# Optimization experiments

Measured on AMD Instinct MI355X. Metric: run time of the kernel, lower is better.

Reference implementation:

```python
import jax, jax.numpy as jnp
import numpy as np

N = 100000      # nodes
E = 1600000     # edges (avg degree 16)
D = 128         # in = hid = out dim


def setup_inputs() -> dict:
    key = jax.random.key(0)
    ks = jax.random.split(key, 7)
    x = jax.random.normal(ks[0], (N, D), dtype=jnp.float32)
    src = jax.random.randint(ks[1], (E,), 0, N, dtype=jnp.int32)
    dst = jax.random.randint(ks[2], (E,), 0, N, dtype=jnp.int32)
    s = 1.0 / np.sqrt(2 * D)  # torch Linear default init bound
    W0 = jax.random.uniform(ks[3], (D, 2 * D), jnp.float32, -s, s)
    b0 = jax.random.uniform(ks[4], (D,), jnp.float32, -s, s)
    W1 = jax.random.uniform(ks[5], (D, 2 * D), jnp.float32, -s, s)
    b1 = jax.random.uniform(ks[6], (D,), jnp.float32, -s, s)
    return {"x": x, "src": src, "dst": dst, "W0": W0, "b0": b0, "W1": W1, "b1": b1}


def graph_conv_left(x, src, dst):
    """DGL GraphConv(norm='left', weight=False, bias=False):
    h_v = sum_{(u->v) in E} x_u / max(outdeg(u), 1)."""
    n = x.shape[0]
    deg = jax.ops.segment_sum(jnp.ones_like(src, dtype=x.dtype), src, num_segments=n)
    deg = jnp.maximum(deg, 1.0)
    msgs = (x / deg[:, None])[src]          # [E, D] gather of normalized src feats
    return jax.ops.segment_sum(msgs, dst, num_segments=n)  # [N, D] scatter-add


def reference(x, src, dst, W0, b0, W1, b1):
    # layer 0: concat(self, agg) -> linear -> relu
    h = jnp.concatenate([x, graph_conv_left(x, src, dst)], axis=1)  # [N, 2D]
    h = jax.nn.relu(h @ W0.T + b0)                                  # [N, D]
    # layer 1 (output): concat -> linear (no relu)
    out = jnp.concatenate([h, graph_conv_left(h, src, dst)], axis=1) @ W1.T + b1
    return out
```

## Files before the change

kernel.cpp:

```cpp
#include <hip/hip_runtime.h>
#include <hip/hip_fp16.h>

#define DIM 128
#define CAP 64
#define BW_LOG 8
#define BW_NODES 256
#define CHUNK_P 4096
#define KCELL 40
#define MAXCHUNK 512
#define WSTRIDE 264

typedef _Float16 f16x8 __attribute__((ext_vector_type(8)));
typedef float f32x4 __attribute__((ext_vector_type(4)));
typedef unsigned int uint;

__global__ __launch_bounds__(512) void k_front(const int* __restrict__ src,
                                               const int* __restrict__ dst,
                                               uint* __restrict__ dbuf,
                                               uint* __restrict__ sbuf,
                                               uint* __restrict__ cntD,
                                               uint* __restrict__ cntS,
                                               const float* __restrict__ W0,
                                               const float* __restrict__ W1,
                                               const float* __restrict__ x,
                                               __half* __restrict__ Wh0,
                                               __half* __restrict__ Wh1,
                                               __half* __restrict__ fh,
                                               int E, int NB, int nchunk, int nquadX) {
    if ((int)blockIdx.x >= nchunk) {
        int i = ((int)blockIdx.x - nchunk) * 512 + threadIdx.x;
        const float* in; __half* out; int q;
        if (i < 8192)        { in = W0; out = Wh0; q = i; }
        else if (i < 16384)  { in = W1; out = Wh1; q = i - 8192; }
        else {
            q = i - 16384;
            if (q >= nquadX) return;
            in = x; out = fh;
        }
        float4 v = ((const float4*)in)[q];
        __half2* o = (__half2*)out;
        o[q * 2]     = __floats2half2_rn(v.x, v.y);
        o[q * 2 + 1] = __floats2half2_rn(v.z, v.w);
        return;
    }
    extern __shared__ uint smem[];
    uint* rb    = smem;
    uint* cells = smem + NB;
    int blk = blockIdx.x;
    int e0 = blk * CHUNK_P;

    int4 sv[2], dv[2];
    bool ok[2];
#pragma unroll
    for (int q = 0; q < 2; ++q) {
        int i4 = (e0 >> 2) + q * 512 + (int)threadIdx.x;
        int e = i4 << 2;
        ok[q] = (e < E);
        if (ok[q]) {
            sv[q] = ((const int4*)src)[i4];
            dv[q] = ((const int4*)dst)[i4];
        }
    }

    const int KQ = KCELL / 4;
    int nq = NB * KQ;

    for (int i = threadIdx.x; i < NB; i += 512) rb[i] = 0;
    __syncthreads();
#pragma unroll
    for (int q = 0; q < 2; ++q) {
        if (!ok[q]) continue;
        int ds[4] = {dv[q].x, dv[q].y, dv[q].z, dv[q].w};
        int ss[4] = {sv[q].x, sv[q].y, sv[q].z, sv[q].w};
#pragma unroll
        for (int k = 0; k < 4; ++k) {
            uint d = (uint)ds[k];
            uint bd = d >> BW_LOG;
            uint r = atomicAdd(&rb[bd], 1);
            if (r < KCELL)
                cells[bd * KCELL + r] = ((d & (BW_NODES - 1)) << 17) | (uint)ss[k];
        }
    }
    __syncthreads();
    for (int u = threadIdx.x; u < nq; u += 512) {
        int bucket = u / KQ;
        int s4 = u - bucket * KQ;
        ((uint4*)dbuf)[((size_t)bucket * nchunk + blk) * KQ + s4] = ((const uint4*)cells)[u];
    }
    for (int i = threadIdx.x; i < NB; i += 512) {
        uint c = rb[i];
        cntD[(uint)i * nchunk + blk] = c < KCELL ? c : KCELL;
    }
    __syncthreads();

    for (int i = threadIdx.x; i < NB; i += 512) rb[i] = 0;
    __syncthreads();
#pragma unroll
    for (int q = 0; q < 2; ++q) {
        if (!ok[q]) continue;
        int ss[4] = {sv[q].x, sv[q].y, sv[q].z, sv[q].w};
#pragma unroll
        for (int k = 0; k < 4; ++k) {
            uint s = (uint)ss[k];
            uint bs = s >> BW_LOG;
            uint r = atomicAdd(&rb[bs], 1);
            if (r < KCELL)
                cells[bs * KCELL + r] = s;
        }
    }
    __syncthreads();
    for (int u = threadIdx.x; u < nq; u += 512) {
        int bucket = u / KQ;
        int s4 = u - bucket * KQ;
        ((uint4*)sbuf)[((size_t)bucket * nchunk + blk) * KQ + s4] = ((const uint4*)cells)[u];
    }
    for (int i = threadIdx.x; i < NB; i += 512) {
        uint c = rb[i];
        cntS[(uint)i * nchunk + blk] = c < KCELL ? c : KCELL;
    }
}

__global__ __launch_bounds__(512) void k_build(const uint* __restrict__ dbuf,
                                               const uint* __restrict__ cntD,
                                               const uint* __restrict__ sbuf,
                                               const uint* __restrict__ cntS,
                                               int* __restrict__ edge_pad,
                                               int* __restrict__ cnt,
                                               float* __restrict__ invd,
                                               int N, int NB, int nchunk) {
    __shared__ uint mcell[MAXCHUNK];
    __shared__ uint cur[BW_NODES];
    __shared__ int  img[128 * CAP];
    int gid = blockIdx.x;
    if (gid < NB) {
        int b = gid;
        for (int c = threadIdx.x; c < nchunk; c += 512)
            mcell[c] = cntD[(uint)b * nchunk + c];
        uint base = (uint)b * nchunk * KCELL;
        int total = nchunk * KCELL;
        int node0 = b << BW_LOG;
        for (int g = 0; g < 2; ++g) {
            int l0 = g << 7;
            for (int i = threadIdx.x; i < 128; i += 512) cur[i] = 0;
            __syncthreads();
            uint v[4]; bool val[4];
            for (int sb = 0; sb < total; sb += 2048) {
#pragma unroll
                for (int q = 0; q < 4; ++q) {
                    int s = sb + q * 512 + (int)threadIdx.x;
                    val[q] = false;
                    if (s < total) {
                        int c = s / KCELL;
                        int j = s - c * KCELL;
                        if ((uint)j < mcell[c]) { val[q] = true; v[q] = dbuf[base + s]; }
                    }
                }
#pragma unroll
                for (int q = 0; q < 4; ++q) {
                    if (val[q]) {
                        uint local = v[q] >> 17;
                        if ((int)(local >> 7) == g) {
                            uint slot = atomicAdd(&cur[local - l0], 1);
                            if (slot < CAP)
                                img[(local - l0) * CAP + slot] = (int)(v[q] & 0x1FFFFu);
                        }
                    }
                }
            }
            __syncthreads();
            int4* gp = (int4*)&edge_pad[(size_t)(node0 + l0) * CAP];
            const int4* lp = (const int4*)img;
            for (int i = threadIdx.x; i < 128 * CAP / 4; i += 512) {
                int row = i >> 4;
                if (node0 + l0 + row < N) gp[i] = lp[i];
            }
            for (int i = threadIdx.x; i < 128; i += 512) {
                int node = node0 + l0 + i;
                if (node < N) cnt[node] = (int)(cur[i] < CAP ? cur[i] : CAP);
            }
            __syncthreads();
        }
    } else {
        int b = gid - NB;
        for (int c = threadIdx.x; c < nchunk; c += 512)
            mcell[c] = cntS[(uint)b * nchunk + c];
        for (int i = threadIdx.x; i < BW_NODES; i += 512) cur[i] = 0;
        __syncthreads();
        uint base = (uint)b * nchunk * KCELL;
        int total = nchunk * KCELL;
        uint v[4]; bool val[4];
        for (int sb = 0; sb < total; sb += 2048) {
#pragma unroll
            for (int q = 0; q < 4; ++q) {
                int s = sb + q * 512 + (int)threadIdx.x;
                val[q] = false;
                if (s < total) {
                    int c = s / KCELL;
                    int j = s - c * KCELL;
                    if ((uint)j < mcell[c]) { val[q] = true; v[q] = sbuf[base + s]; }
                }
            }
#pragma unroll
            for (int q = 0; q < 4; ++q)
                if (val[q]) atomicAdd(&cur[v[q] & (BW_NODES - 1)], 1);
        }
        __syncthreads();
        int node0 = b << BW_LOG;
        for (int i = threadIdx.x; i < BW_NODES; i += 512) {
            int node = node0 + i;
            if (node < N) {
                uint d = cur[i];
                invd[node] = 1.0f / (float)(d > 1u ? d : 1u);
            }
        }
    }
}

__global__ __launch_bounds__(256) void k_gather(const __half* __restrict__ feat,
                                                const float* __restrict__ invd,
                                                const int* __restrict__ edge_pad,
                                                const int* __restrict__ cnt_arr,
                                                __half* __restrict__ agg, int n) {
    int v = blockIdx.x * 4 + (threadIdx.x >> 6);
    int lane = threadIdx.x & 63;
    int quad = lane >> 4;
    int lq   = lane & 15;
    if (v >= n) return;
    int cnt = cnt_arr[v];
    if (cnt > CAP) cnt = CAP;

    int u_lane = 0;
    float w_lane = 0.f;
    if (lane < cnt) {
        u_lane = edge_pad[(size_t)v * CAP + lane];
        w_lane = invd[u_lane];
    }

    float acc[8] = {0.f, 0.f, 0.f, 0.f, 0.f, 0.f, 0.f, 0.f};
    int cntUp = (cnt + 7) & ~7;
    for (int j = 0; j < cntUp; j += 8) {
        int   ua = __shfl(u_lane, j + quad);
        float wa = __shfl(w_lane, j + quad);
        int   ub = __shfl(u_lane, j + 4 + quad);
        float wb = __shfl(w_lane, j + 4 + quad);
        uint4 ra = *(const uint4*)&feat[(size_t)ua * 128 + lq * 8];
        uint4 rb = *(const uint4*)&feat[(size_t)ub * 128 + lq * 8];
        const __half2* pa = (const __half2*)&ra;
        const __half2* pb = (const __half2*)&rb;
#pragma unroll
        for (int i = 0; i < 4; ++i) {
            float2 fa = __half22float2(pa[i]);
            float2 fb = __half22float2(pb[i]);
            acc[2 * i]     = fmaf(fa.x, wa, acc[2 * i]);
            acc[2 * i + 1] = fmaf(fa.y, wa, acc[2 * i + 1]);
            acc[2 * i]     = fmaf(fb.x, wb, acc[2 * i]);
            acc[2 * i + 1] = fmaf(fb.y, wb, acc[2 * i + 1]);
        }
    }
#pragma unroll
    for (int off = 16; off <= 32; off <<= 1) {
#pragma unroll
        for (int i = 0; i < 8; ++i) acc[i] += __shfl_xor(acc[i], off);
    }
    if (quad == 0) {
        __half2 o[4];
#pragma unroll
        for (int i = 0; i < 4; ++i) o[i] = __floats2half2_rn(acc[2 * i], acc[2 * i + 1]);
        *(uint4*)&agg[(size_t)v * 128 + lq * 8] = *(const uint4*)o;
    }
}

template <bool RELU, bool OUT16>
__global__ __launch_bounds__(256) void k_gemm_f16(const _Float16* __restrict__ A0,
                                                  const _Float16* __restrict__ A1,
                                                  const _Float16* __restrict__ Wh,
                                                  const float* __restrict__ bias,
                                                  float* __restrict__ out32,
                                                  _Float16* __restrict__ out16,
                                                  int n_rows) {
    __shared__ _Float16 Ws[64 * WSTRIDE];
    int tid  = threadIdx.x;
    int wave = tid >> 6;
    int lane = tid & 63;
    int quad = lane >> 4;
    int l16  = lane & 15;

    int u = blockIdx.x;
    int full = (int)gridDim.x & ~15;
    int mb, half;
    if (u < full) { mb = (u >> 4) * 8 + (u & 7); half = (u >> 3) & 1; }
    else {
        int rem = ((int)gridDim.x >> 1) - (full >> 1);
        int t = u - full;
        mb = (full >> 1) + t % rem;
        half = t / rem;
    }
    int n0 = half * 64;
    int m0 = mb * 128 + wave * 32;

#pragma unroll
    for (int i = 0; i < 8; ++i) {
        int chunk = i * 256 + tid;
        int r = chunk >> 5;
        int c = (chunk & 31) * 8;
        *(f16x8*)&Ws[r * WSTRIDE + c] = *(const f16x8*)&Wh[(n0 + r) * 256 + c];
    }
    __syncthreads();

    f32x4 acc[2][4] = {};

    int ra = m0 + l16;
    int rb = m0 + 16 + l16;
    size_t r0 = (size_t)(ra < n_rows ? ra : 0);
    size_t r1 = (size_t)(rb < n_rows ? rb : 0);

#pragma unroll
    for (int ks = 0; ks < 8; ++ks) {
        int k0 = ks * 32;
        const _Float16* Ab = (k0 < 128) ? A0 : A1;
        int kk = (k0 & 127) + quad * 8;
        f16x8 a0 = *(const f16x8*)&Ab[r0 * 128 + kk];
        f16x8 a1 = *(const f16x8*)&Ab[r1 * 128 + kk];
        f16x8 b[4];
#pragma unroll
        for (int t = 0; t < 4; ++t)
            b[t] = *(const f16x8*)&Ws[(t * 16 + l16) * WSTRIDE + k0 + quad * 8];
#pragma unroll
        for (int t = 0; t < 4; ++t) {
            acc[0][t] = __builtin_amdgcn_mfma_f32_16x16x32_f16(a0, b[t], acc[0][t], 0, 0, 0);
            acc[1][t] = __builtin_amdgcn_mfma_f32_16x16x32_f16(a1, b[t], acc[1][t], 0, 0, 0);
        }
    }

#pragma unroll
    for (int t = 0; t < 4; ++t) {
        int col = n0 + t * 16 + l16;
        float bv = bias[col];
#pragma unroll
        for (int g = 0; g < 2; ++g) {
#pragma unroll
            for (int r = 0; r < 4; ++r) {
                int row = m0 + g * 16 + quad * 4 + r;
                if (row < n_rows) {
                    float v = acc[g][t][r] + bv;
                    if (RELU) v = fmaxf(v, 0.f);
                    if (OUT16) out16[(size_t)row * 128 + col] = (_Float16)v;
                    else       out32[(size_t)row * 128 + col] = v;
                }
            }
        }
    }
}

extern "C" void kernel_launch(void* const* d_in, const int* in_sizes, int n_in,
                              void* d_out, int out_size, void* d_ws, size_t ws_size,
                              hipStream_t stream) {
    const float* x  = (const float*)d_in[0];
    const int*   src = (const int*)d_in[1];
    const int*   dst = (const int*)d_in[2];
    const float* W0 = (const float*)d_in[3];
    const float* b0 = (const float*)d_in[4];
    const float* W1 = (const float*)d_in[5];
    const float* b1 = (const float*)d_in[6];
    int N = in_sizes[0] / DIM;
    int E = in_sizes[1];
    float* out = (float*)d_out;
    int NB = (N + BW_NODES - 1) >> BW_LOG;
    int nchunk = (E + CHUNK_P - 1) / CHUNK_P;
    size_t ncell = (size_t)NB * nchunk;
    size_t cellWords = ncell * KCELL;

    char* p = (char*)d_ws;
    uint* cntDc = (uint*)p; p += (ncell * 4 + 63) & ~(size_t)63;
    uint* cntSc = (uint*)p; p += (ncell * 4 + 63) & ~(size_t)63;
    int*   edge_pad = (int*)p;   p += (size_t)N * CAP * 4;
    int*   cnt  = (int*)p;  p += ((size_t)N * 4 + 63) & ~(size_t)63;
    float* invd = (float*)p; p += ((size_t)N * 4 + 63) & ~(size_t)63;
    char*  uni = p;
    size_t featB = (size_t)N * DIM * 2;
    size_t cellB = cellWords * 4;
    size_t uniSz = cellB > featB ? cellB : featB;
    p += (uniSz + 63) & ~(size_t)63;
    uint*   dbuf = (uint*)uni;
    __half* aggh = (__half*)uni;
    __half* fh   = (__half*)p; p += featB;
    char*  uni2 = p; p += (uniSz + 63) & ~(size_t)63;
    uint*   sbuf = (uint*)uni2;
    __half* hh   = (__half*)uni2;
    __half* Wh0  = (__half*)p; p += 128 * 256 * 2;
    __half* Wh1  = (__half*)p; p += 128 * 256 * 2;
    (void)ws_size; (void)n_in; (void)out_size;

    int nquadX = N * DIM / 4;
    int gP = (16384 + nquadX + 511) / 512;
    size_t shScatter = (size_t)(NB + NB * KCELL) * 4;
    k_front<<<nchunk + gP, 512, shScatter, stream>>>(src, dst, dbuf, sbuf, cntDc, cntSc,
                                                     W0, W1, x, Wh0, Wh1, fh,
                                                     E, NB, nchunk, nquadX);

    k_build<<<2 * NB, 512, 0, stream>>>(dbuf, cntDc, sbuf, cntSc,
                                        edge_pad, cnt, invd, N, NB, nchunk);

    int gG = (N + 3) / 4;
    int gM = 2 * ((N + 127) / 128);

    k_gather<<<gG, 256, 0, stream>>>(fh, invd, edge_pad, cnt, aggh, N);
    k_gemm_f16<true, true><<<gM, 256, 0, stream>>>((const _Float16*)fh, (const _Float16*)aggh,
                                                   (const _Float16*)Wh0, b0,
                                                   nullptr, (_Float16*)hh, N);

    k_gather<<<gG, 256, 0, stream>>>(hh, invd, edge_pad, cnt, aggh, N);
    k_gemm_f16<false, false><<<gM, 256, 0, stream>>>((const _Float16*)hh, (const _Float16*)aggh,
                                                     (const _Float16*)Wh1, b1,
                                                     out, nullptr, N);
}
```

Measured before the change: 316.6 us.

## Fuse neighbor gather with MFMA linear layer, prepermute weights into fragment layout

Merges the per-node gather kernel and the GEMM kernel into one kernel per layer: each wave aggregates 16 nodes into shared memory and then runs MFMA over the concatenated self and aggregate features against all 128 output columns. Weights are pre-permuted at conversion time into the MFMA B-fragment order, so they are read straight from global memory without LDS staging. This removes the aggregate buffer round trip through global memory and two launches. In exchange, gather parallelism per block drops because each wave handles its 16 nodes serially, and every wave re-reads the full weight matrix from global or cache.

New measurement: 348.3 us. 1.1x slower.

```diff
diff --git a/kernel.cpp b/kernel.cpp
--- a/kernel.cpp
+++ b/kernel.cpp
@@ -8,7 +8,6 @@
 #define CHUNK_P 4096
 #define KCELL 40
 #define MAXCHUNK 512
-#define WSTRIDE 264
 
 typedef _Float16 f16x8 __attribute__((ext_vector_type(8)));
 typedef float f32x4 __attribute__((ext_vector_type(4)));
@@ -23,22 +22,35 @@
                                                const float* __restrict__ W0,
                                                const float* __restrict__ W1,
                                                const float* __restrict__ x,
-                                               __half* __restrict__ Wh0,
-                                               __half* __restrict__ Wh1,
+                                               _Float16* __restrict__ Wr0,
+                                               _Float16* __restrict__ Wr1,
                                                __half* __restrict__ fh,
                                                int E, int NB, int nchunk, int nquadX) {
     if ((int)blockIdx.x >= nchunk) {
         int i = ((int)blockIdx.x - nchunk) * 512 + threadIdx.x;
-        const float* in; __half* out; int q;
-        if (i < 8192)        { in = W0; out = Wh0; q = i; }
-        else if (i < 16384)  { in = W1; out = Wh1; q = i - 8192; }
-        else {
-            q = i - 16384;
-            if (q >= nquadX) return;
-            in = x; out = fh;
-        }
-        float4 v = ((const float4*)in)[q];
-        __half2* o = (__half2*)out;
+        if (i < 8192) {
+            const float* W = (i < 4096) ? W0 : W1;
+            _Float16* Wr  = (i < 4096) ? Wr0 : Wr1;
+            int j = i & 4095;
+            int f = j >> 6;
+            int ln = j & 63;
+            int ks = f >> 3, t = f & 7;
+            int col = t * 16 + (ln & 15);
+            int k0 = ks * 32 + (ln >> 4) * 8;
+            const float* wsrc = W + (size_t)col * 256 + k0;
+            float4 va = *(const float4*)wsrc;
+            float4 vb = *(const float4*)(wsrc + 4);
+            __half2* o = (__half2*)(Wr + ((size_t)f * 64 + ln) * 8);
+            o[0] = __floats2half2_rn(va.x, va.y);
+            o[1] = __floats2half2_rn(va.z, va.w);
+            o[2] = __floats2half2_rn(vb.x, vb.y);
+            o[3] = __floats2half2_rn(vb.z, vb.w);
+            return;
+        }
+        int q = i - 8192;
+        if (q >= nquadX) return;
+        float4 v = ((const float4*)x)[q];
+        __half2* o = (__half2*)fh;
         o[q * 2]     = __floats2half2_rn(v.x, v.y);
         o[q * 2 + 1] = __floats2half2_rn(v.z, v.w);
         return;
@@ -216,137 +228,97 @@
     }
 }
 
-__global__ __launch_bounds__(256) void k_gather(const __half* __restrict__ feat,
-                                                const float* __restrict__ invd,
-                                                const int* __restrict__ edge_pad,
-                                                const int* __restrict__ cnt_arr,
-                                                __half* __restrict__ agg, int n) {
-    int v = blockIdx.x * 4 + (threadIdx.x >> 6);
-    int lane = threadIdx.x & 63;
-    int quad = lane >> 4;
-    int lq   = lane & 15;
-    if (v >= n) return;
-    int cnt = cnt_arr[v];
-    if (cnt > CAP) cnt = CAP;
-
-    int u_lane = 0;
-    float w_lane = 0.f;
-    if (lane < cnt) {
-        u_lane = edge_pad[(size_t)v * CAP + lane];
-        w_lane = invd[u_lane];
-    }
-
-    float acc[8] = {0.f, 0.f, 0.f, 0.f, 0.f, 0.f, 0.f, 0.f};
-    int cntUp = (cnt + 7) & ~7;
-    for (int j = 0; j < cntUp; j += 8) {
-        int   ua = __shfl(u_lane, j + quad);
-        float wa = __shfl(w_lane, j + quad);
-        int   ub = __shfl(u_lane, j + 4 + quad);
-        float wb = __shfl(w_lane, j + 4 + quad);
-        uint4 ra = *(const uint4*)&feat[(size_t)ua * 128 + lq * 8];
-        uint4 rb = *(const uint4*)&feat[(size_t)ub * 128 + lq * 8];
-        const __half2* pa = (const __half2*)&ra;
-        const __half2* pb = (const __half2*)&rb;
-#pragma unroll
-        for (int i = 0; i < 4; ++i) {
-            float2 fa = __half22float2(pa[i]);
-            float2 fb = __half22float2(pb[i]);
-            acc[2 * i]     = fmaf(fa.x, wa, acc[2 * i]);
-            acc[2 * i + 1] = fmaf(fa.y, wa, acc[2 * i + 1]);
-            acc[2 * i]     = fmaf(fb.x, wb, acc[2 * i]);
-            acc[2 * i + 1] = fmaf(fb.y, wb, acc[2 * i + 1]);
-        }
-    }
-#pragma unroll
-    for (int off = 16; off <= 32; off <<= 1) {
-#pragma unroll
-        for (int i = 0; i < 8; ++i) acc[i] += __shfl_xor(acc[i], off);
-    }
-    if (quad == 0) {
-        __half2 o[4];
-#pragma unroll
-        for (int i = 0; i < 4; ++i) o[i] = __floats2half2_rn(acc[2 * i], acc[2 * i + 1]);
-        *(uint4*)&agg[(size_t)v * 128 + lq * 8] = *(const uint4*)o;
-    }
-}
-
 template <bool RELU, bool OUT16>
-__global__ __launch_bounds__(256) void k_gemm_f16(const _Float16* __restrict__ A0,
-                                                  const _Float16* __restrict__ A1,
-                                                  const _Float16* __restrict__ Wh,
-                                                  const float* __restrict__ bias,
-                                                  float* __restrict__ out32,
-                                                  _Float16* __restrict__ out16,
-                                                  int n_rows) {
-    __shared__ _Float16 Ws[64 * WSTRIDE];
+__global__ __launch_bounds__(256) void k_fused(const __half* __restrict__ feat,
+                                               const float* __restrict__ invd,
+                                               const int* __restrict__ edge_pad,
+                                               const int* __restrict__ cnt_arr,
+                                               const _Float16* __restrict__ Wr,
+                                               const float* __restrict__ bias,
+                                               float* __restrict__ out32,
+                                               _Float16* __restrict__ out16,
+                                               int n_rows) {
+    __shared__ _Float16 agg[64 * 136];
     int tid  = threadIdx.x;
     int wave = tid >> 6;
     int lane = tid & 63;
     int quad = lane >> 4;
-    int l16  = lane & 15;
-
-    int u = blockIdx.x;
-    int full = (int)gridDim.x & ~15;
-    int mb, half;
-    if (u < full) { mb = (u >> 4) * 8 + (u & 7); half = (u >> 3) & 1; }
-    else {
-        int rem = ((int)gridDim.x >> 1) - (full >> 1);
-        int t = u - full;
-        mb = (full >> 1) + t % rem;
-        half = t / rem;
-    }
-    int n0 = half * 64;
-    int m0 = mb * 128 + wave * 32;
-
-#pragma unroll
-    for (int i = 0; i < 8; ++i) {
-        int chunk = i * 256 + tid;
-        int r = chunk >> 5;
-        int c = (chunk & 31) * 8;
-        *(f16x8*)&Ws[r * WSTRIDE + c] = *(const f16x8*)&Wh[(n0 + r) * 256 + c];
-    }
-    __syncthreads();
-
-    f32x4 acc[2][4] = {};
-
-    int ra = m0 + l16;
-    int rb = m0 + 16 + l16;
-    size_t r0 = (size_t)(ra < n_rows ? ra : 0);
-    size_t r1 = (size_t)(rb < n_rows ? rb : 0);
-
+    int lq   = lane & 15;
+    int rowbase = blockIdx.x * 64 + wave * 16;
+
+    for (int nn = 0; nn < 16; ++nn) {
+        int v = rowbase + nn;
+        if (v >= n_rows) break;
+        int cnt = cnt_arr[v];
+        if (cnt > CAP) cnt = CAP;
+        int u_lane = 0;
+        float w_lane = 0.f;
+        if (lane < cnt) {
+            u_lane = edge_pad[(size_t)v * CAP + lane];
+            w_lane = invd[u_lane];
+        }
+        float acc[8] = {0.f, 0.f, 0.f, 0.f, 0.f, 0.f, 0.f, 0.f};
+        int cntUp = (cnt + 7) & ~7;
+        for (int j = 0; j < cntUp; j += 8) {
+            int   ua = __shfl(u_lane, j + quad);
+            float wa = __shfl(w_lane, j + quad);
+            int   ub = __shfl(u_lane, j + 4 + quad);
+            float wb = __shfl(w_lane, j + 4 + quad);
+            uint4 ra = *(const uint4*)&feat[(size_t)ua * 128 + lq * 8];
+            uint4 rb = *(const uint4*)&feat[(size_t)ub * 128 + lq * 8];
+            const __half2* pa = (const __half2*)&ra;
+            const __half2* pb = (const __half2*)&rb;
+#pragma unroll
+            for (int i = 0; i < 4; ++i) {
+                float2 fa = __half22float2(pa[i]);
+                float2 fb = __half22float2(pb[i]);
+                acc[2 * i]     = fmaf(fa.x, wa, acc[2 * i]);
+                acc[2 * i + 1] = fmaf(fa.y, wa, acc[2 * i + 1]);
+                acc[2 * i]     = fmaf(fb.x, wb, acc[2 * i]);
+                acc[2 * i + 1] = fmaf(fb.y, wb, acc[2 * i + 1]);
+            }
+        }
+#pragma unroll
+        for (int off = 16; off <= 32; off <<= 1) {
+#pragma unroll
+            for (int i = 0; i < 8; ++i) acc[i] += __shfl_xor(acc[i], off);
+        }
+        if (quad == 0) {
+            __half2 o[4];
+#pragma unroll
+            for (int i = 0; i < 4; ++i) o[i] = __floats2half2_rn(acc[2 * i], acc[2 * i + 1]);
+            *(uint4*)&agg[(wave * 16 + nn) * 136 + lq * 8] = *(const uint4*)o;
+        }
+    }
+
+    f32x4 acc[8] = {};
+    int myrow = rowbase + lq;
+    size_t ar = (size_t)(myrow < n_rows ? myrow : 0);
+    const _Float16* fp = (const _Float16*)feat;
+    int aggoff = (wave * 16 + lq) * 136 + quad * 8;
 #pragma unroll
     for (int ks = 0; ks < 8; ++ks) {
-        int k0 = ks * 32;
-        const _Float16* Ab = (k0 < 128) ? A0 : A1;
-        int kk = (k0 & 127) + quad * 8;
-        f16x8 a0 = *(const f16x8*)&Ab[r0 * 128 + kk];
-        f16x8 a1 = *(const f16x8*)&Ab[r1 * 128 + kk];
-        f16x8 b[4];
-#pragma unroll
-        for (int t = 0; t < 4; ++t)
-            b[t] = *(const f16x8*)&Ws[(t * 16 + l16) * WSTRIDE + k0 + quad * 8];
-#pragma unroll
-        for (int t = 0; t < 4; ++t) {
-            acc[0][t] = __builtin_amdgcn_mfma_f32_16x16x32_f16(a0, b[t], acc[0][t], 0, 0, 0);
-            acc[1][t] = __builtin_amdgcn_mfma_f32_16x16x32_f16(a1, b[t], acc[1][t], 0, 0, 0);
-        }
-    }
-
-#pragma unroll
-    for (int t = 0; t < 4; ++t) {
-        int col = n0 + t * 16 + l16;
+        f16x8 a;
+        if (ks < 4) a = *(const f16x8*)&fp[ar * 128 + ks * 32 + quad * 8];
+        else        a = *(const f16x8*)&agg[aggoff + (ks - 4) * 32];
+#pragma unroll
+        for (int t = 0; t < 8; ++t) {
+            f16x8 b = *(const f16x8*)&Wr[((size_t)((ks * 8 + t) * 64 + lane)) * 8];
+            acc[t] = __builtin_amdgcn_mfma_f32_16x16x32_f16(a, b, acc[t], 0, 0, 0);
+        }
+    }
+#pragma unroll
+    for (int t = 0; t < 8; ++t) {
+        int col = t * 16 + lq;
         float bv = bias[col];
 #pragma unroll
-        for (int g = 0; g < 2; ++g) {
-#pragma unroll
-            for (int r = 0; r < 4; ++r) {
-                int row = m0 + g * 16 + quad * 4 + r;
-                if (row < n_rows) {
-                    float v = acc[g][t][r] + bv;
-                    if (RELU) v = fmaxf(v, 0.f);
-                    if (OUT16) out16[(size_t)row * 128 + col] = (_Float16)v;
-                    else       out32[(size_t)row * 128 + col] = v;
-                }
+        for (int r = 0; r < 4; ++r) {
+            int row = rowbase + quad * 4 + r;
+            if (row < n_rows) {
+                float v = acc[t][r] + bv;
+                if (RELU) v = fmaxf(v, 0.f);
+                if (OUT16) out16[(size_t)row * 128 + col] = (_Float16)v;
+                else       out32[(size_t)row * 128 + col] = v;
             }
         }
     }
@@ -376,41 +348,34 @@
     int*   edge_pad = (int*)p;   p += (size_t)N * CAP * 4;
     int*   cnt  = (int*)p;  p += ((size_t)N * 4 + 63) & ~(size_t)63;
     float* invd = (float*)p; p += ((size_t)N * 4 + 63) & ~(size_t)63;
-    char*  uni = p;
     size_t featB = (size_t)N * DIM * 2;
     size_t cellB = cellWords * 4;
     size_t uniSz = cellB > featB ? cellB : featB;
-    p += (uniSz + 63) & ~(size_t)63;
+    char*  uni = p; p += (uniSz + 63) & ~(size_t)63;
     uint*   dbuf = (uint*)uni;
-    __half* aggh = (__half*)uni;
     __half* fh   = (__half*)p; p += featB;
     char*  uni2 = p; p += (uniSz + 63) & ~(size_t)63;
     uint*   sbuf = (uint*)uni2;
     __half* hh   = (__half*)uni2;
-    __half* Wh0  = (__half*)p; p += 128 * 256 * 2;
-    __half* Wh1  = (__half*)p; p += 128 * 256 * 2;
+    _Float16* Wr0 = (_Float16*)p; p += 64 * 64 * 8 * 2;
+    _Float16* Wr1 = (_Float16*)p; p += 64 * 64 * 8 * 2;
     (void)ws_size; (void)n_in; (void)out_size;
 
     int nquadX = N * DIM / 4;
-    int gP = (16384 + nquadX + 511) / 512;
+    int gP = (8192 + nquadX + 511) / 512;
     size_t shScatter = (size_t)(NB + NB * KCELL) * 4;
     k_front<<<nchunk + gP, 512, shScatter, stream>>>(src, dst, dbuf, sbuf, cntDc, cntSc,
-                                                     W0, W1, x, Wh0, Wh1, fh,
+                                                     W0, W1, x, Wr0, Wr1, fh,
                                                      E, NB, nchunk, nquadX);
 
     k_build<<<2 * NB, 512, 0, stream>>>(dbuf, cntDc, sbuf, cntSc,
                                         edge_pad, cnt, invd, N, NB, nchunk);
 
-    int gG = (N + 3) / 4;
-    int gM = 2 * ((N + 127) / 128);
-
-    k_gather<<<gG, 256, 0, stream>>>(fh, invd, edge_pad, cnt, aggh, N);
-    k_gemm_f16<true, true><<<gM, 256, 0, stream>>>((const _Float16*)fh, (const _Float16*)aggh,
-                                                   (const _Float16*)Wh0, b0,
-                                                   nullptr, (_Float16*)hh, N);
-
-    k_gather<<<gG, 256, 0, stream>>>(hh, invd, edge_pad, cnt, aggh, N);
-    k_gemm_f16<false, false><<<gM, 256, 0, stream>>>((const _Float16*)hh, (const _Float16*)aggh,
-                                                     (const _Float16*)Wh1, b1,
-                                                     out, nullptr, N);
+    int gF = (N + 63) / 64;
+
+    k_fused<true, true><<<gF, 256, 0, stream>>>(fh, invd, edge_pad, cnt,
+                                                Wr0, b0, nullptr, (_Float16*)hh, N);
+
+    k_fused<false, false><<<gF, 256, 0, stream>>>(hh, invd, edge_pad, cnt,
+                                                  Wr1, b1, out, nullptr, N);
 }
```

## Compress source-degree cells to bytes and compute full output width per GEMM block

Applied to the files above, without the earlier changes.

The source-bucket cells now hold only the low 8 bits of each node id (one byte per entry, padded to 48 per cell). This cuts the global traffic the front kernel writes and the degree-counting build pass reads, and the build pass unpacks four entries per word. The GEMM kernel now has each block compute both 64-column halves of the output, loading the A rows once into registers and restaging W in shared memory twice. That halves A reads and the grid size, at the cost of higher register pressure and an extra barrier-separated weight load.

Result: slower. 328.5 us (+3.8%).

```diff
diff --git a/kernel.cpp b/kernel.cpp
--- a/kernel.cpp
+++ b/kernel.cpp
@@ -7,12 +7,14 @@
 #define BW_NODES 256
 #define CHUNK_P 4096
 #define KCELL 40
+#define KCB   48
 #define MAXCHUNK 512
 #define WSTRIDE 264
 
 typedef _Float16 f16x8 __attribute__((ext_vector_type(8)));
 typedef float f32x4 __attribute__((ext_vector_type(4)));
 typedef unsigned int uint;
+typedef unsigned char uchar;
 
 __global__ __launch_bounds__(512) void k_front(const int* __restrict__ src,
                                                const int* __restrict__ dst,
@@ -44,8 +46,10 @@
         return;
     }
     extern __shared__ uint smem[];
-    uint* rb    = smem;
-    uint* cells = smem + NB;
+    int NBa = (NB + 3) & ~3;
+    uint*  rb     = smem;
+    uint*  cells  = smem + NBa;
+    uchar* cellsB = (uchar*)(smem + NBa);
     int blk = blockIdx.x;
     int e0 = blk * CHUNK_P;
 
@@ -105,14 +109,16 @@
             uint bs = s >> BW_LOG;
             uint r = atomicAdd(&rb[bs], 1);
             if (r < KCELL)
-                cells[bs * KCELL + r] = s;
+                cellsB[bs * KCB + r] = (uchar)(s & (BW_NODES - 1));
         }
     }
     __syncthreads();
-    for (int u = threadIdx.x; u < nq; u += 512) {
-        int bucket = u / KQ;
-        int s4 = u - bucket * KQ;
-        ((uint4*)sbuf)[((size_t)bucket * nchunk + blk) * KQ + s4] = ((const uint4*)cells)[u];
+    const int KQS = KCB / 16;
+    int nqS = NB * KQS;
+    for (int u = threadIdx.x; u < nqS; u += 512) {
+        int bucket = u / KQS;
+        int s4 = u - bucket * KQS;
+        ((uint4*)sbuf)[((size_t)bucket * nchunk + blk) * KQS + s4] = ((const uint4*)cellsB)[u];
     }
     for (int i = threadIdx.x; i < NB; i += 512) {
         uint c = rb[i];
@@ -186,23 +192,33 @@
             mcell[c] = cntS[(uint)b * nchunk + c];
         for (int i = threadIdx.x; i < BW_NODES; i += 512) cur[i] = 0;
         __syncthreads();
-        uint base = (uint)b * nchunk * KCELL;
-        int total = nchunk * KCELL;
-        uint v[4]; bool val[4];
-        for (int sb = 0; sb < total; sb += 2048) {
+        const uint* sbU = sbuf + (size_t)b * nchunk * (KCB / 4);
+        int totalU = nchunk * (KCB / 4);
+        uint w[4]; int cc[4], jb[4]; bool val[4];
+        for (int su = 0; su < totalU; su += 2048) {
 #pragma unroll
             for (int q = 0; q < 4; ++q) {
-                int s = sb + q * 512 + (int)threadIdx.x;
+                int s = su + q * 512 + (int)threadIdx.x;
                 val[q] = false;
-                if (s < total) {
-                    int c = s / KCELL;
-                    int j = s - c * KCELL;
-                    if ((uint)j < mcell[c]) { val[q] = true; v[q] = sbuf[base + s]; }
+                if (s < totalU) {
+                    int c = s / (KCB / 4);
+                    int j = (s - c * (KCB / 4)) * 4;
+                    if ((uint)j < mcell[c]) {
+                        val[q] = true; w[q] = sbU[s]; cc[q] = c; jb[q] = j;
+                    }
                 }
             }
 #pragma unroll
-            for (int q = 0; q < 4; ++q)
-                if (val[q]) atomicAdd(&cur[v[q] & (BW_NODES - 1)], 1);
+            for (int q = 0; q < 4; ++q) {
+                if (val[q]) {
+                    uint m = mcell[cc[q]];
+                    uint ww = w[q];
+#pragma unroll
+                    for (int i = 0; i < 4; ++i)
+                        if ((uint)(jb[q] + i) < m)
+                            atomicAdd(&cur[(ww >> (8 * i)) & 255u], 1);
+                }
+            }
         }
         __syncthreads();
         int node0 = b << BW_LOG;
@@ -284,68 +300,67 @@
     int lane = tid & 63;
     int quad = lane >> 4;
     int l16  = lane & 15;
-
-    int u = blockIdx.x;
-    int full = (int)gridDim.x & ~15;
-    int mb, half;
-    if (u < full) { mb = (u >> 4) * 8 + (u & 7); half = (u >> 3) & 1; }
-    else {
-        int rem = ((int)gridDim.x >> 1) - (full >> 1);
-        int t = u - full;
-        mb = (full >> 1) + t % rem;
-        half = t / rem;
-    }
-    int n0 = half * 64;
-    int m0 = mb * 128 + wave * 32;
-
-#pragma unroll
-    for (int i = 0; i < 8; ++i) {
-        int chunk = i * 256 + tid;
-        int r = chunk >> 5;
-        int c = (chunk & 31) * 8;
-        *(f16x8*)&Ws[r * WSTRIDE + c] = *(const f16x8*)&Wh[(n0 + r) * 256 + c];
-    }
-    __syncthreads();
-
-    f32x4 acc[2][4] = {};
+    int m0 = blockIdx.x * 128 + wave * 32;
 
     int ra = m0 + l16;
     int rb = m0 + 16 + l16;
     size_t r0 = (size_t)(ra < n_rows ? ra : 0);
     size_t r1 = (size_t)(rb < n_rows ? rb : 0);
 
+    f16x8 a0[8], a1[8];
 #pragma unroll
     for (int ks = 0; ks < 8; ++ks) {
-        int k0 = ks * 32;
-        const _Float16* Ab = (k0 < 128) ? A0 : A1;
-        int kk = (k0 & 127) + quad * 8;
-        f16x8 a0 = *(const f16x8*)&Ab[r0 * 128 + kk];
-        f16x8 a1 = *(const f16x8*)&Ab[r1 * 128 + kk];
-        f16x8 b[4];
-#pragma unroll
-        for (int t = 0; t < 4; ++t)
-            b[t] = *(const f16x8*)&Ws[(t * 16 + l16) * WSTRIDE + k0 + quad * 8];
+        const _Float16* Ab = (ks < 4) ? A0 : A1;
+        int kk = (ks & 3) * 32 + quad * 8;
+        a0[ks] = *(const f16x8*)&Ab[r0 * 128 + kk];
+        a1[ks] = *(const f16x8*)&Ab[r1 * 128 + kk];
+    }
+
+    f32x4 acc[2][8] = {};
+#pragma unroll
+    for (int h = 0; h < 2; ++h) {
+        int n0 = h * 64;
+        __syncthreads();
+#pragma unroll
+        for (int i = 0; i < 8; ++i) {
+            int chunk = i * 256 + tid;
+            int r = chunk >> 5;
+            int c = (chunk & 31) * 8;
+            *(f16x8*)&Ws[r * WSTRIDE + c] = *(const f16x8*)&Wh[(n0 + r) * 256 + c];
+        }
+        __syncthreads();
+#pragma unroll
+        for (int ks = 0; ks < 8; ++ks) {
+            int k0 = ks * 32;
+            f16x8 b[4];
+#pragma unroll
+            for (int t = 0; t < 4; ++t)
+                b[t] = *(const f16x8*)&Ws[(t * 16 + l16) * WSTRIDE + k0 + quad * 8];
+#pragma unroll
+            for (int t = 0; t < 4; ++t) {
+                acc[0][h * 4 + t] = __builtin_amdgcn_mfma_f32_16x16x32_f16(a0[ks], b[t], acc[0][h * 4 + t], 0, 0, 0);
+                acc[1][h * 4 + t] = __builtin_amdgcn_mfma_f32_16x16x32_f16(a1[ks], b[t], acc[1][h * 4 + t], 0, 0, 0);
+            }
+        }
+    }
+
+#pragma unroll
+    for (int h = 0; h < 2; ++h) {
 #pragma unroll
         for (int t = 0; t < 4; ++t) {
-            acc[0][t] = __builtin_amdgcn_mfma_f32_16x16x32_f16(a0, b[t], acc[0][t], 0, 0, 0);
-            acc[1][t] = __builtin_amdgcn_mfma_f32_16x16x32_f16(a1, b[t], acc[1][t], 0, 0, 0);
-        }
-    }
-
-#pragma unroll
-    for (int t = 0; t < 4; ++t) {
-        int col = n0 + t * 16 + l16;
-        float bv = bias[col];
-#pragma unroll
-        for (int g = 0; g < 2; ++g) {
-#pragma unroll
-            for (int r = 0; r < 4; ++r) {
-                int row = m0 + g * 16 + quad * 4 + r;
-                if (row < n_rows) {
-                    float v = acc[g][t][r] + bv;
-                    if (RELU) v = fmaxf(v, 0.f);
-                    if (OUT16) out16[(size_t)row * 128 + col] = (_Float16)v;
-                    else       out32[(size_t)row * 128 + col] = v;
+            int col = h * 64 + t * 16 + l16;
+            float bv = bias[col];
+#pragma unroll
+            for (int g = 0; g < 2; ++g) {
+#pragma unroll
+                for (int r = 0; r < 4; ++r) {
+                    int row = m0 + g * 16 + quad * 4 + r;
+                    if (row < n_rows) {
+                        float v = acc[g][h * 4 + t][r] + bv;
+                        if (RELU) v = fmaxf(v, 0.f);
+                        if (OUT16) out16[(size_t)row * 128 + col] = (_Float16)v;
+                        else       out32[(size_t)row * 128 + col] = v;
+                    }
                 }
             }
         }
@@ -368,32 +383,33 @@
     int NB = (N + BW_NODES - 1) >> BW_LOG;
     int nchunk = (E + CHUNK_P - 1) / CHUNK_P;
     size_t ncell = (size_t)NB * nchunk;
-    size_t cellWords = ncell * KCELL;
 
     char* p = (char*)d_ws;
-    uint* cntDc = (uint*)p; p += (ncell * 4 + 63) & ~(size_t)63;
-    uint* cntSc = (uint*)p; p += (ncell * 4 + 63) & ~(size_t)63;
-    int*   edge_pad = (int*)p;   p += (size_t)N * CAP * 4;
-    int*   cnt  = (int*)p;  p += ((size_t)N * 4 + 63) & ~(size_t)63;
-    float* invd = (float*)p; p += ((size_t)N * 4 + 63) & ~(size_t)63;
-    char*  uni = p;
-    size_t featB = (size_t)N * DIM * 2;
-    size_t cellB = cellWords * 4;
-    size_t uniSz = cellB > featB ? cellB : featB;
-    p += (uniSz + 63) & ~(size_t)63;
+    uint* cntDc = (uint*)p; p += (ncell * sizeof(uint) + 63) & ~(size_t)63;
+    uint* cntSc = (uint*)p; p += (ncell * sizeof(uint) + 63) & ~(size_t)63;
+    int*   edge_pad = (int*)p;   p += (size_t)N * CAP * sizeof(int);
+    int*   cnt  = (int*)p;  p += ((size_t)N * sizeof(int) + 63) & ~(size_t)63;
+    float* invd = (float*)p; p += ((size_t)N * sizeof(float) + 63) & ~(size_t)63;
+    size_t featB = (size_t)N * DIM * sizeof(__half);
+    size_t dbufB = ncell * KCELL * sizeof(uint);
+    size_t sbufB = ncell * KCB;
+    size_t uni1Sz = dbufB > featB ? dbufB : featB;
+    size_t uni2Sz = sbufB > featB ? sbufB : featB;
+    char*  uni = p; p += (uni1Sz + 63) & ~(size_t)63;
     uint*   dbuf = (uint*)uni;
     __half* aggh = (__half*)uni;
     __half* fh   = (__half*)p; p += featB;
-    char*  uni2 = p; p += (uniSz + 63) & ~(size_t)63;
+    char*  uni2 = p; p += (uni2Sz + 63) & ~(size_t)63;
     uint*   sbuf = (uint*)uni2;
     __half* hh   = (__half*)uni2;
-    __half* Wh0  = (__half*)p; p += 128 * 256 * 2;
-    __half* Wh1  = (__half*)p; p += 128 * 256 * 2;
+    __half* Wh0  = (__half*)p; p += 128 * 256 * sizeof(__half);
+    __half* Wh1  = (__half*)p; p += 128 * 256 * sizeof(__half);
     (void)ws_size; (void)n_in; (void)out_size;
 
     int nquadX = N * DIM / 4;
     int gP = (16384 + nquadX + 511) / 512;
-    size_t shScatter = (size_t)(NB + NB * KCELL) * 4;
+    int NBa = (NB + 3) & ~3;
+    size_t shScatter = (size_t)(NBa + NB * KCELL) * sizeof(uint);
     k_front<<<nchunk + gP, 512, shScatter, stream>>>(src, dst, dbuf, sbuf, cntDc, cntSc,
                                                      W0, W1, x, Wh0, Wh1, fh,
                                                      E, NB, nchunk, nquadX);
@@ -402,7 +418,7 @@
                                         edge_pad, cnt, invd, N, NB, nchunk);
 
     int gG = (N + 3) / 4;
-    int gM = 2 * ((N + 127) / 128);
+    int gM = (N + 127) / 128;
 
     k_gather<<<gG, 256, 0, stream>>>(fh, invd, edge_pad, cnt, aggh, N);
     k_gemm_f16<true, true><<<gM, 256, 0, stream>>>((const _Float16*)fh, (const _Float16*)aggh,
```
